# Kernel optimization log

Hardware: AMD Instinct MI355X
Metric: run time of the kernel (lower is better)

The kernel has to match this reference:

```python
import jax, jax.numpy as jnp
import numpy as np

EMBED_SIZE = 100
HEAD_SIZE = 64
B, T = 4, 4096


def setup_inputs() -> dict:
    key = jax.random.key(0)
    k1, k2, k3, k4 = jax.random.split(key, 4)
    x = jax.random.normal(k1, (B, T, EMBED_SIZE), dtype=jnp.float32)
    Wq = jax.random.normal(k2, (EMBED_SIZE, HEAD_SIZE), dtype=jnp.float32) * 0.1
    Wk = jax.random.normal(k3, (EMBED_SIZE, HEAD_SIZE), dtype=jnp.float32) * 0.1
    Wv = jax.random.normal(k4, (EMBED_SIZE, HEAD_SIZE), dtype=jnp.float32) * 0.1
    return {"x": x, "Wq": Wq, "Wk": Wk, "Wv": Wv}


def reference(x, Wq, Wk, Wv):
    # Projections (bias-free Linear): [B, T, head_size]
    q = x @ Wq
    k = x @ Wk
    v = x @ Wv
    scale = HEAD_SIZE ** (-0.5)
    # Scaled scores [B, T, T]
    scores = jnp.einsum("bqd,bkd->bqk", q, k) * scale
    # Faithful to source: tril the scores, then mask entries that equal 0 to -inf
    masked = jnp.tril(scores)
    masked = jnp.where(masked == 0, -jnp.inf, masked)
    attn = jax.nn.softmax(masked, axis=-1)
    out = jnp.einsum("bqk,bkd->bqd", attn, v)  # [B, T, head_size]
    return out
```

## Files before the change

### kernel.cpp

```cpp
#include <hip/hip_runtime.h>
#include <hip/hip_bf16.h>
#include <stdint.h>

#define NB 4
#define NT 4096
#define NE 100
#define ND 64

typedef __attribute__((ext_vector_type(8))) short short8;
typedef __attribute__((ext_vector_type(4))) short short4_;
typedef __attribute__((ext_vector_type(4))) float float4_;
typedef unsigned short ushort_t;

__device__ __forceinline__ unsigned short f2bf(float f) {
  union { float f; uint32_t u; } v; v.f = f;
  uint32_t u = v.u;
  u += 0x7fffu + ((u >> 16) & 1u);
  return (unsigned short)(u >> 16);
}

__device__ __forceinline__ float bf2f(short us) {
  union { uint32_t u; float f; } v;
  v.u = ((uint32_t)(unsigned short)us) << 16;
  return v.f;
}

__device__ __forceinline__ float fast_exp2(float x) {
#if __has_builtin(__builtin_amdgcn_exp2f)
  return __builtin_amdgcn_exp2f(x);
#else
  return exp2f(x);
#endif
}

__global__ __launch_bounds__(256) void proj_kernel(
    const float* __restrict__ x, const float* __restrict__ Wq,
    const float* __restrict__ Wk, const float* __restrict__ Wv,
    ushort_t* __restrict__ Qb, ushort_t* __restrict__ Kb,
    ushort_t* __restrict__ Vt) {
  __shared__ __align__(16) float xs[64 * NE];
  __shared__ __align__(16) ushort_t Wl[3][25][64][4];
  __shared__ __align__(16) ushort_t Vl[64][72];

  const int tid = threadIdx.x;
  const int r0  = blockIdx.x * 64;

  {
    const float4_* xsrc = (const float4_*)(x + (size_t)r0 * NE);
    float4_* xdst = (float4_*)xs;
    for (int i = tid; i < 1600; i += 256) xdst[i] = xsrc[i];
  }
  {
    const int ch = tid >> 6, d = tid & 63;
    if (ch < 3) {
      const float* Ws = (ch == 0) ? Wq : (ch == 1) ? Wk : Wv;
      #pragma unroll 5
      for (int qd = 0; qd < 25; ++qd) {
        short4_ pk;
        #pragma unroll
        for (int jj = 0; jj < 4; ++jj)
          pk[jj] = (short)f2bf(Ws[(4*qd + jj)*ND + d]);
        *(short4_*)&Wl[ch][qd][d][0] = pk;
      }
    }
  }
  __syncthreads();

  const int wv = tid >> 6, lane = tid & 63;
  const float QS = 0.125f * 1.44269504088896340736f;

  for (int it = 0; it < 4; ++it) {
    float aq[4] = {0,0,0,0}, ak[4] = {0,0,0,0}, av[4] = {0,0,0,0};
    const float* xw = xs + (it*16 + wv*4) * NE;
    for (int qd = 0; qd < 25; ++qd) {
      short4_ w4q = *(const short4_*)&Wl[0][qd][lane][0];
      short4_ w4k = *(const short4_*)&Wl[1][qd][lane][0];
      short4_ w4v = *(const short4_*)&Wl[2][qd][lane][0];
      float4_ x0 = *(const float4_*)&xw[0*NE + 4*qd];
      float4_ x1 = *(const float4_*)&xw[1*NE + 4*qd];
      float4_ x2 = *(const float4_*)&xw[2*NE + 4*qd];
      float4_ x3 = *(const float4_*)&xw[3*NE + 4*qd];
      #pragma unroll
      for (int jj = 0; jj < 4; ++jj) {
        float fq = bf2f(w4q[jj]), fk = bf2f(w4k[jj]), fv = bf2f(w4v[jj]);
        aq[0] += x0[jj]*fq; ak[0] += x0[jj]*fk; av[0] += x0[jj]*fv;
        aq[1] += x1[jj]*fq; ak[1] += x1[jj]*fk; av[1] += x1[jj]*fv;
        aq[2] += x2[jj]*fq; ak[2] += x2[jj]*fk; av[2] += x2[jj]*fv;
        aq[3] += x3[jj]*fq; ak[3] += x3[jj]*fk; av[3] += x3[jj]*fv;
      }
    }
    #pragma unroll
    for (int j = 0; j < 4; ++j) {
      int lrow = it*16 + wv*4 + j;
      int row  = r0 + lrow;
      Qb[(size_t)row*ND + lane] = f2bf(aq[j] * QS);
      Kb[(size_t)row*ND + lane] = f2bf(ak[j]);
      Vl[lrow][lane] = f2bf(av[j]);
    }
  }
  __syncthreads();

  {
    const int b = r0 >> 12, r0t = r0 & (NT - 1);
    for (int i = tid; i < 512; i += 256) {
      int d = i >> 3, seg = i & 7;
      short8 pk;
      #pragma unroll
      for (int k2 = 0; k2 < 8; ++k2) pk[k2] = (short)Vl[seg*8 + k2][d];
      *(short8*)(Vt + ((size_t)(b*ND + d))*NT + r0t + seg*8) = pk;
    }
  }
}

__global__ __launch_bounds__(512) void attn_kernel(
    const ushort_t* __restrict__ Qb, const ushort_t* __restrict__ Kb,
    const ushort_t* __restrict__ Vt, float* __restrict__ out) {
  extern __shared__ __align__(16) char arena[];
  ushort_t* KsB = (ushort_t*)arena;
  ushort_t* VsB = KsB + 4*2*4096;
  ushort_t* PbB = VsB + 4*2*4096;
  float*    Om  = (float*)arena;
  float*    Ml  = (float*)(arena + 131072);

  const int tid  = threadIdx.x;
  const int w    = tid >> 6, lane = tid & 63;
  const int pp   = w >> 1, h = w & 1;
  const int qrow = lane & 15, grp = lane >> 4;
  const int srow8 = lane >> 3, sc16 = lane & 7;

  const int blk = blockIdx.x;
  const int xcd = blk & 7;
  const int b   = xcd >> 1;
  const int p   = ((blk >> 3) << 1) | (xcd & 1);

  const ushort_t* Kbase = Kb + (size_t)b*NT*ND;
  const ushort_t* Vtb   = Vt + (size_t)b*ND*NT;

  ushort_t* Ks0 = KsB + pp*8192;
  ushort_t* Vs0 = VsB + pp*8192;
  ushort_t* Pw  = PbB + w*1152;

  for (int phase = 0; phase < 2; ++phase) {
    const int g  = phase ? p : (127 - p);
    const int q0 = g << 5;
    const int nt = (g >> 1) + 1;
    const int qglob = q0 + h*16 + qrow;

    const ushort_t* Qr = Qb + ((size_t)(b*NT + q0 + h*16 + qrow))*ND + 8*grp;
    const short8 qf0 = *(const short8*)(Qr);
    const short8 qf1 = *(const short8*)(Qr + 32);

    float4_ O0 = {0,0,0,0}, O1 = {0,0,0,0}, O2 = {0,0,0,0}, O3 = {0,0,0,0};
    float m = -1e30f, lsum = 0.f;
    short8 sr[8];

    const int maxIter = (nt + 3) >> 2;

    if (pp < nt) {
      const int kv0 = pp << 6;
      #pragma unroll
      for (int i = 0; i < 8; ++i) {
        int row = 8*i + srow8;
        sr[i] = (h == 0)
          ? *(const short8*)(Kbase + (size_t)(kv0 + row)*ND + sc16*8)
          : *(const short8*)(Vtb + (size_t)row*NT + kv0 + sc16*8);
      }
      ushort_t* dst = (h == 0) ? Ks0 : Vs0;
      #pragma unroll
      for (int i = 0; i < 8; ++i) {
        int row = 8*i + srow8;
        *(short8*)&dst[row*64 + ((sc16 ^ (row & 7)) << 3)] = sr[i];
      }
    }
    __syncthreads();

    for (int it = 0; it < maxIter; ++it) {
      const int t    = pp + (it << 2);
      const int buf  = it & 1;
      const bool act = (t < nt);
      const bool hasNext = act && (t + 4 < nt);

      if (hasNext) {
        const int kn0 = (t + 4) << 6;
        #pragma unroll
        for (int i = 0; i < 8; ++i) {
          int row = 8*i + srow8;
          sr[i] = (h == 0)
            ? *(const short8*)(Kbase + (size_t)(kn0 + row)*ND + sc16*8)
            : *(const short8*)(Vtb + (size_t)row*NT + kn0 + sc16*8);
        }
      }

      if (act) {
        const int kv0 = t << 6;
        const ushort_t* Kc = Ks0 + buf*4096;
        const ushort_t* Vc = Vs0 + buf*4096;

        float4_ sA[4];
        #pragma unroll
        for (int st = 0; st < 4; ++st) {
          int row = st*16 + qrow;
          short8 kf0 = *(const short8*)&Kc[row*64 + (((grp    ) ^ (row & 7)) << 3)];
          short8 kf1 = *(const short8*)&Kc[row*64 + (((grp + 4) ^ (row & 7)) << 3)];
          float4_ acc = {0,0,0,0};
          acc = __builtin_amdgcn_mfma_f32_16x16x32_bf16(kf0, qf0, acc, 0,0,0);
          acc = __builtin_amdgcn_mfma_f32_16x16x32_bf16(kf1, qf1, acc, 0,0,0);
          sA[st] = acc;
        }

        short8 vf[8];
        #pragma unroll
        for (int j = 0; j < 4; ++j) {
          int row = j*16 + qrow;
          vf[2*j]   = *(const short8*)&Vc[row*64 + (((grp    ) ^ (row & 7)) << 3)];
          vf[2*j+1] = *(const short8*)&Vc[row*64 + (((grp + 4) ^ (row & 7)) << 3)];
        }

        if (t == nt - 1) {
          #pragma unroll
          for (int st = 0; st < 4; ++st)
            #pragma unroll
            for (int r = 0; r < 4; ++r) {
              int kv = kv0 + st*16 + grp*4 + r;
              if (kv > qglob) sA[st][r] = -1e30f;
            }
        }

        float pmax = sA[0][0];
        #pragma unroll
        for (int st = 0; st < 4; ++st)
          #pragma unroll
          for (int r = 0; r < 4; ++r) pmax = fmaxf(pmax, sA[st][r]);
        if (!__all(pmax <= m + 8.0f)) {
          float tm = pmax;
          tm = fmaxf(tm, __shfl_xor(tm, 16));
          tm = fmaxf(tm, __shfl_xor(tm, 32));
          const float mnew  = fmaxf(m, tm);
          const float alpha = fast_exp2(m - mnew);
          m = mnew;
          lsum *= alpha;
          #pragma unroll
          for (int r = 0; r < 4; ++r) {
            float ar = __shfl(alpha, grp*4 + r);
            O0[r] *= ar; O1[r] *= ar; O2[r] *= ar; O3[r] *= ar;
          }
        }

        float psum = 0.f;
        #pragma unroll
        for (int st = 0; st < 4; ++st) {
          short4_ pv;
          #pragma unroll
          for (int r = 0; r < 4; ++r) {
            float pe = fast_exp2(sA[st][r] - m);
            psum += pe;
            pv[r] = (short)f2bf(pe);
          }
          *(short4_*)&Pw[qrow*72 + st*16 + grp*4] = pv;
        }
        psum += __shfl_xor(psum, 16);
        psum += __shfl_xor(psum, 32);
        lsum += psum;

        asm volatile("s_waitcnt lgkmcnt(0)" ::: "memory");

        const short8 pf0 = *(const short8*)&Pw[qrow*72 + 8*grp];
        const short8 pf1 = *(const short8*)&Pw[qrow*72 + 32 + 8*grp];
        O0 = __builtin_amdgcn_mfma_f32_16x16x32_bf16(pf0, vf[0], O0, 0,0,0);
        O0 = __builtin_amdgcn_mfma_f32_16x16x32_bf16(pf1, vf[1], O0, 0,0,0);
        O1 = __builtin_amdgcn_mfma_f32_16x16x32_bf16(pf0, vf[2], O1, 0,0,0);
        O1 = __builtin_amdgcn_mfma_f32_16x16x32_bf16(pf1, vf[3], O1, 0,0,0);
        O2 = __builtin_amdgcn_mfma_f32_16x16x32_bf16(pf0, vf[4], O2, 0,0,0);
        O2 = __builtin_amdgcn_mfma_f32_16x16x32_bf16(pf1, vf[5], O2, 0,0,0);
        O3 = __builtin_amdgcn_mfma_f32_16x16x32_bf16(pf0, vf[6], O3, 0,0,0);
        O3 = __builtin_amdgcn_mfma_f32_16x16x32_bf16(pf1, vf[7], O3, 0,0,0);
      }

      if (hasNext) {
        ushort_t* dst = ((h == 0) ? Ks0 : Vs0) + (buf ^ 1)*4096;
        #pragma unroll
        for (int i = 0; i < 8; ++i) {
          int row = 8*i + srow8;
          *(short8*)&dst[row*64 + ((sc16 ^ (row & 7)) << 3)] = sr[i];
        }
      }
      __syncthreads();
    }

    #pragma unroll
    for (int r = 0; r < 4; ++r) {
      int row = grp*4 + r;
      Om[w*1024 + row*64 + 0*16 + qrow] = O0[r];
      Om[w*1024 + row*64 + 1*16 + qrow] = O1[r];
      Om[w*1024 + row*64 + 2*16 + qrow] = O2[r];
      Om[w*1024 + row*64 + 3*16 + qrow] = O3[r];
    }
    if (lane < 16) {
      Ml[(w*16 + lane)*2]     = m;
      Ml[(w*16 + lane)*2 + 1] = lsum;
    }
    __syncthreads();

    for (int i = tid; i < 2048; i += 512) {
      int row = i >> 6, d = i & 63;
      int hh = row >> 4, r16 = row & 15;
      float M = -3e30f;
      #pragma unroll
      for (int p2 = 0; p2 < 4; ++p2)
        M = fmaxf(M, Ml[((2*p2 + hh)*16 + r16)*2]);
      float ls = 0.f, os = 0.f;
      #pragma unroll
      for (int p2 = 0; p2 < 4; ++p2) {
        int w2 = 2*p2 + hh;
        float sc = fast_exp2(Ml[(w2*16 + r16)*2] - M);
        ls += sc * Ml[(w2*16 + r16)*2 + 1];
        os += sc * Om[w2*1024 + r16*64 + d];
      }
      out[((size_t)b*NT + q0 + row)*ND + d] = os / ls;
    }
    __syncthreads();
  }
}

extern "C" void kernel_launch(void* const* d_in, const int* in_sizes, int n_in,
                              void* d_out, int out_size, void* d_ws, size_t ws_size,
                              hipStream_t stream) {
  const float* x  = (const float*)d_in[0];
  const float* Wq = (const float*)d_in[1];
  const float* Wk = (const float*)d_in[2];
  const float* Wv = (const float*)d_in[3];
  float* out = (float*)d_out;

  ushort_t* Qb = (ushort_t*)d_ws;
  ushort_t* Kb = Qb + (size_t)NB*NT*ND;
  ushort_t* Vt = Kb + (size_t)NB*NT*ND;

  const int ldsBytes = (4*2*4096 + 4*2*4096 + 8*16*72) * 2;
  static bool attrSet = false;
  (void)attrSet;
  hipFuncSetAttribute((const void*)attn_kernel,
                      hipFuncAttributeMaxDynamicSharedMemorySize, ldsBytes);

  proj_kernel<<<dim3(256), dim3(256), 0, stream>>>(x, Wq, Wk, Wv, Qb, Kb, Vt);
  attn_kernel<<<dim3(256), dim3(512), ldsBytes, stream>>>(Qb, Kb, Vt, out);
}
```

Before: 124.9 us.

## Load K and V fragments directly from global into registers, drop LDS staging

```diff
diff --git a/kernel.cpp b/kernel.cpp
--- a/kernel.cpp
+++ b/kernel.cpp
@@ -112,21 +112,17 @@
   }
 }
 
-__global__ __launch_bounds__(512) void attn_kernel(
+__global__ __launch_bounds__(512, 2) void attn_kernel(
     const ushort_t* __restrict__ Qb, const ushort_t* __restrict__ Kb,
     const ushort_t* __restrict__ Vt, float* __restrict__ out) {
-  extern __shared__ __align__(16) char arena[];
-  ushort_t* KsB = (ushort_t*)arena;
-  ushort_t* VsB = KsB + 4*2*4096;
-  ushort_t* PbB = VsB + 4*2*4096;
-  float*    Om  = (float*)arena;
-  float*    Ml  = (float*)(arena + 131072);
+  __shared__ __align__(16) ushort_t Pb[8][16][72];
+  __shared__ __align__(16) float Om[8][16][64];
+  __shared__ float Ml[8][16][2];
 
   const int tid  = threadIdx.x;
   const int w    = tid >> 6, lane = tid & 63;
   const int pp   = w >> 1, h = w & 1;
   const int qrow = lane & 15, grp = lane >> 4;
-  const int srow8 = lane >> 3, sc16 = lane & 7;
 
   const int blk = blockIdx.x;
   const int xcd = blk & 7;
@@ -135,10 +131,7 @@
 
   const ushort_t* Kbase = Kb + (size_t)b*NT*ND;
   const ushort_t* Vtb   = Vt + (size_t)b*ND*NT;
-
-  ushort_t* Ks0 = KsB + pp*8192;
-  ushort_t* Vs0 = VsB + pp*8192;
-  ushort_t* Pw  = PbB + w*1152;
+  ushort_t* Pw = &Pb[w][0][0];
 
   for (int phase = 0; phase < 2; ++phase) {
     const int g  = phase ? p : (127 - p);
@@ -152,68 +145,52 @@
 
     float4_ O0 = {0,0,0,0}, O1 = {0,0,0,0}, O2 = {0,0,0,0}, O3 = {0,0,0,0};
     float m = -1e30f, lsum = 0.f;
-    short8 sr[8];
+    short8 kc[8], kn[8];
 
     const int maxIter = (nt + 3) >> 2;
 
     if (pp < nt) {
       const int kv0 = pp << 6;
       #pragma unroll
-      for (int i = 0; i < 8; ++i) {
-        int row = 8*i + srow8;
-        sr[i] = (h == 0)
-          ? *(const short8*)(Kbase + (size_t)(kv0 + row)*ND + sc16*8)
-          : *(const short8*)(Vtb + (size_t)row*NT + kv0 + sc16*8);
-      }
-      ushort_t* dst = (h == 0) ? Ks0 : Vs0;
-      #pragma unroll
-      for (int i = 0; i < 8; ++i) {
-        int row = 8*i + srow8;
-        *(short8*)&dst[row*64 + ((sc16 ^ (row & 7)) << 3)] = sr[i];
-      }
-    }
-    __syncthreads();
+      for (int st = 0; st < 4; ++st) {
+        const ushort_t* kp = Kbase + (size_t)(kv0 + st*16 + qrow)*ND + 8*grp;
+        kc[2*st]   = *(const short8*)(kp);
+        kc[2*st+1] = *(const short8*)(kp + 32);
+      }
+    }
+    #pragma unroll
+    for (int i = 0; i < 8; ++i) kn[i] = kc[i];
 
     for (int it = 0; it < maxIter; ++it) {
-      const int t    = pp + (it << 2);
-      const int buf  = it & 1;
+      const int t   = pp + (it << 2);
       const bool act = (t < nt);
-      const bool hasNext = act && (t + 4 < nt);
-
-      if (hasNext) {
-        const int kn0 = (t + 4) << 6;
-        #pragma unroll
-        for (int i = 0; i < 8; ++i) {
-          int row = 8*i + srow8;
-          sr[i] = (h == 0)
-            ? *(const short8*)(Kbase + (size_t)(kn0 + row)*ND + sc16*8)
-            : *(const short8*)(Vtb + (size_t)row*NT + kn0 + sc16*8);
-        }
-      }
-
       if (act) {
         const int kv0 = t << 6;
-        const ushort_t* Kc = Ks0 + buf*4096;
-        const ushort_t* Vc = Vs0 + buf*4096;
+
+        short8 vf[8];
+        #pragma unroll
+        for (int j = 0; j < 4; ++j) {
+          const ushort_t* vp = Vtb + (size_t)(j*16 + qrow)*NT + kv0 + 8*grp;
+          vf[2*j]   = *(const short8*)(vp);
+          vf[2*j+1] = *(const short8*)(vp + 32);
+        }
+        if (t + 4 < nt) {
+          const int kn0 = (t + 4) << 6;
+          #pragma unroll
+          for (int st = 0; st < 4; ++st) {
+            const ushort_t* kp = Kbase + (size_t)(kn0 + st*16 + qrow)*ND + 8*grp;
+            kn[2*st]   = *(const short8*)(kp);
+            kn[2*st+1] = *(const short8*)(kp + 32);
+          }
+        }
 
         float4_ sA[4];
         #pragma unroll
         for (int st = 0; st < 4; ++st) {
-          int row = st*16 + qrow;
-          short8 kf0 = *(const short8*)&Kc[row*64 + (((grp    ) ^ (row & 7)) << 3)];
-          short8 kf1 = *(const short8*)&Kc[row*64 + (((grp + 4) ^ (row & 7)) << 3)];
           float4_ acc = {0,0,0,0};
-          acc = __builtin_amdgcn_mfma_f32_16x16x32_bf16(kf0, qf0, acc, 0,0,0);
-          acc = __builtin_amdgcn_mfma_f32_16x16x32_bf16(kf1, qf1, acc, 0,0,0);
+          acc = __builtin_amdgcn_mfma_f32_16x16x32_bf16(kc[2*st],   qf0, acc, 0,0,0);
+          acc = __builtin_amdgcn_mfma_f32_16x16x32_bf16(kc[2*st+1], qf1, acc, 0,0,0);
           sA[st] = acc;
-        }
-
-        short8 vf[8];
-        #pragma unroll
-        for (int j = 0; j < 4; ++j) {
-          int row = j*16 + qrow;
-          vf[2*j]   = *(const short8*)&Vc[row*64 + (((grp    ) ^ (row & 7)) << 3)];
-          vf[2*j+1] = *(const short8*)&Vc[row*64 + (((grp + 4) ^ (row & 7)) << 3)];
         }
 
         if (t == nt - 1) {
@@ -246,21 +223,20 @@
           }
         }
 
-        float psum = 0.f;
+        float ps0 = 0.f, ps1 = 0.f;
         #pragma unroll
         for (int st = 0; st < 4; ++st) {
           short4_ pv;
-          #pragma unroll
-          for (int r = 0; r < 4; ++r) {
-            float pe = fast_exp2(sA[st][r] - m);
-            psum += pe;
-            pv[r] = (short)f2bf(pe);
-          }
+          float pe0 = fast_exp2(sA[st][0] - m);
+          float pe1 = fast_exp2(sA[st][1] - m);
+          float pe2 = fast_exp2(sA[st][2] - m);
+          float pe3 = fast_exp2(sA[st][3] - m);
+          pv[0] = (short)f2bf(pe0); pv[1] = (short)f2bf(pe1);
+          pv[2] = (short)f2bf(pe2); pv[3] = (short)f2bf(pe3);
+          ps0 += pe0 + pe1; ps1 += pe2 + pe3;
           *(short4_*)&Pw[qrow*72 + st*16 + grp*4] = pv;
         }
-        psum += __shfl_xor(psum, 16);
-        psum += __shfl_xor(psum, 32);
-        lsum += psum;
+        lsum += ps0 + ps1;
 
         asm volatile("s_waitcnt lgkmcnt(0)" ::: "memory");
 
@@ -274,30 +250,26 @@
         O2 = __builtin_amdgcn_mfma_f32_16x16x32_bf16(pf1, vf[5], O2, 0,0,0);
         O3 = __builtin_amdgcn_mfma_f32_16x16x32_bf16(pf0, vf[6], O3, 0,0,0);
         O3 = __builtin_amdgcn_mfma_f32_16x16x32_bf16(pf1, vf[7], O3, 0,0,0);
-      }
-
-      if (hasNext) {
-        ushort_t* dst = ((h == 0) ? Ks0 : Vs0) + (buf ^ 1)*4096;
-        #pragma unroll
-        for (int i = 0; i < 8; ++i) {
-          int row = 8*i + srow8;
-          *(short8*)&dst[row*64 + ((sc16 ^ (row & 7)) << 3)] = sr[i];
-        }
-      }
-      __syncthreads();
-    }
+
+        #pragma unroll
+        for (int i = 0; i < 8; ++i) kc[i] = kn[i];
+      }
+    }
+
+    lsum += __shfl_xor(lsum, 16);
+    lsum += __shfl_xor(lsum, 32);
 
     #pragma unroll
     for (int r = 0; r < 4; ++r) {
       int row = grp*4 + r;
-      Om[w*1024 + row*64 + 0*16 + qrow] = O0[r];
-      Om[w*1024 + row*64 + 1*16 + qrow] = O1[r];
-      Om[w*1024 + row*64 + 2*16 + qrow] = O2[r];
-      Om[w*1024 + row*64 + 3*16 + qrow] = O3[r];
+      Om[w][row][0*16 + qrow] = O0[r];
+      Om[w][row][1*16 + qrow] = O1[r];
+      Om[w][row][2*16 + qrow] = O2[r];
+      Om[w][row][3*16 + qrow] = O3[r];
     }
     if (lane < 16) {
-      Ml[(w*16 + lane)*2]     = m;
-      Ml[(w*16 + lane)*2 + 1] = lsum;
+      Ml[w][lane][0] = m;
+      Ml[w][lane][1] = lsum;
     }
     __syncthreads();
 
@@ -307,14 +279,14 @@
       float M = -3e30f;
       #pragma unroll
       for (int p2 = 0; p2 < 4; ++p2)
-        M = fmaxf(M, Ml[((2*p2 + hh)*16 + r16)*2]);
+        M = fmaxf(M, Ml[2*p2 + hh][r16][0]);
       float ls = 0.f, os = 0.f;
       #pragma unroll
       for (int p2 = 0; p2 < 4; ++p2) {
         int w2 = 2*p2 + hh;
-        float sc = fast_exp2(Ml[(w2*16 + r16)*2] - M);
-        ls += sc * Ml[(w2*16 + r16)*2 + 1];
-        os += sc * Om[w2*1024 + r16*64 + d];
+        float sc = fast_exp2(Ml[w2][r16][0] - M);
+        ls += sc * Ml[w2][r16][1];
+        os += sc * Om[w2][r16][d];
       }
       out[((size_t)b*NT + q0 + row)*ND + d] = os / ls;
     }
@@ -335,12 +307,6 @@
   ushort_t* Kb = Qb + (size_t)NB*NT*ND;
   ushort_t* Vt = Kb + (size_t)NB*NT*ND;
 
-  const int ldsBytes = (4*2*4096 + 4*2*4096 + 8*16*72) * 2;
-  static bool attrSet = false;
-  (void)attrSet;
-  hipFuncSetAttribute((const void*)attn_kernel,
-                      hipFuncAttributeMaxDynamicSharedMemorySize, ldsBytes);
-
   proj_kernel<<<dim3(256), dim3(256), 0, stream>>>(x, Wq, Wk, Wv, Qb, Kb, Vt);
-  attn_kernel<<<dim3(256), dim3(512), ldsBytes, stream>>>(Qb, Kb, Vt, out);
-}
+  attn_kernel<<<dim3(256), dim3(512), 0, stream>>>(Qb, Kb, Vt, out);
+}
```

Result: slower. 148.8 us (+19.2%).
